# Performance work log

Hardware: AMD Instinct MI355X
Metric: run time of the kernel (lower is better)

The kernel has to match this reference:

```python
import jax, jax.numpy as jnp
import numpy as np

EPS = 1e-08

def _compute_W(V, C, eps=EPS):
    # W = H_k ... H_1, applied sequentially as in the torch loop
    W = jnp.eye(C, dtype=V.dtype)
    def step(W, v):
        v = v / (jnp.linalg.norm(v) + eps)
        # H @ W = W - 2 v (v^T W)
        W = W - 2.0 * jnp.outer(v, v @ W)
        return W, None
    W, _ = jax.lax.scan(step, W, V)
    return W

def setup_inputs() -> dict:
    key = jax.random.key(0)
    k1, k2 = jax.random.split(key)
    x = jax.random.normal(k1, (16, 512, 64, 64), dtype=jnp.float32)
    V = jax.random.normal(k2, (32, 512), dtype=jnp.float32)
    return {"x": x, "V": V}

def reference(x, V):
    B, C, H, Wd = x.shape
    W = _compute_W(V, C)  # [C, C] orthogonal
    # 1x1 conv: out[b,o,h,w] = sum_c W[o,c] * x[b,c,h,w]
    return jnp.einsum('oc,bchw->bohw', W, x)
```

## Files before the change

### kernel.cpp

```cpp
#include <hip/hip_runtime.h>
#include <hip/hip_bf16.h>
#include <stdint.h>
#include <stddef.h>

#define HH_EPS 1e-8f

typedef __attribute__((ext_vector_type(8))) short short8;
typedef __attribute__((ext_vector_type(4))) float f32x4;

#define CDIM 512
#define SDIM 4096
#define BN 128
#define BK 32
#define NSTEP 16

__device__ __forceinline__ size_t wt_idx(int o, int c) {
    return ((((size_t)(c >> 5) * 4 + (o >> 7)) * 8 + ((o >> 4) & 7)) * 64
            + (size_t)((c >> 3) & 3) * 16 + (o & 15)) * 8 + (c & 7);
}

__global__ void compute_w(const float* __restrict__ V,
                          __hip_bfloat16* __restrict__ Wt) {
    const int wave = threadIdx.x >> 6;
    const int lane = threadIdx.x & 63;
    const int jA = (blockIdx.x * 4 + wave) * 2;
    const int jB = jA + 1;
    const int ib = lane * 8;

    float wA[8], wB[8];
    #pragma unroll
    for (int r = 0; r < 8; r++) {
        wA[r] = (ib + r == jA) ? 1.0f : 0.0f;
        wB[r] = (ib + r == jB) ? 1.0f : 0.0f;
    }
    float4 c0 = *(const float4*)(V + ib);
    float4 c1 = *(const float4*)(V + ib + 4);

    for (int k = 0; k < 32; k++) {
        const float v[8] = {c0.x, c0.y, c0.z, c0.w, c1.x, c1.y, c1.z, c1.w};
        if (k < 31) {
            c0 = *(const float4*)(V + (size_t)(k + 1) * 512 + ib);
            c1 = *(const float4*)(V + (size_t)(k + 1) * 512 + ib + 4);
        }
        float dA = 0.0f, dB = 0.0f, ss = 0.0f;
        #pragma unroll
        for (int r = 0; r < 8; r++) {
            dA += v[r] * wA[r];
            dB += v[r] * wB[r];
            ss += v[r] * v[r];
        }
        #pragma unroll
        for (int off = 32; off > 0; off >>= 1) {
            dA += __shfl_xor(dA, off);
            dB += __shfl_xor(dB, off);
            ss += __shfl_xor(ss, off);
        }
        const float t = sqrtf(ss) + HH_EPS;
        const float scale = 2.0f / (t * t);
        const float tA = scale * dA, tB = scale * dB;
        #pragma unroll
        for (int r = 0; r < 8; r++) {
            wA[r] -= tA * v[r];
            wB[r] -= tB * v[r];
        }
    }
    #pragma unroll
    for (int r = 0; r < 8; r++) {
        Wt[wt_idx(ib + r, jA)] = __float2bfloat16(wA[r]);
        Wt[wt_idx(ib + r, jB)] = __float2bfloat16(wB[r]);
    }
}

__device__ __forceinline__ void gld_lds16(const void* g, void* l) {
    __builtin_amdgcn_global_load_lds(
        (const __attribute__((address_space(1))) uint32_t*)g,
        (__attribute__((address_space(3))) uint32_t*)l, 16, 0, 0);
}

template<int N> __device__ __forceinline__ void wait_vm() {
    __builtin_amdgcn_s_waitcnt((N & 15) | ((N >> 4) << 14) | (7 << 4) | (15 << 8));
}

__device__ __forceinline__ void lds_barrier() {
    __builtin_amdgcn_s_waitcnt(0xC07F);
    __builtin_amdgcn_s_barrier();
}

constexpr int vm_pre(int kt) { return (kt + 4 < NSTEP) ? 8 : 0; }

__global__ __launch_bounds__(512, 2) void hh_gemm(
    const float* __restrict__ x,
    const __hip_bfloat16* __restrict__ Wt,
    float* __restrict__ out)
{
    __shared__ __attribute__((aligned(16))) __hip_bfloat16 Albuf[2][CDIM * BK];
    __shared__ __attribute__((aligned(16))) __hip_bfloat16 Bbuf[2][BN * BK];

    const int tid  = threadIdx.x;
    const int wave = tid >> 6, lane = tid & 63;
    const int ow = wave & 3, nh = wave >> 2;
    const int quad = lane >> 4, l16 = lane & 15;

    const int bid = blockIdx.x;
    const int b   = bid >> 5;
    const int nt  = bid & 31;
    const int n0  = nt * BN;

    const float* xb = x + (size_t)b * CDIM * SDIM;
    const int bn = tid & 127;
    const int kq = tid >> 7;
    const float* xp0 = xb + (size_t)(kq * 8) * SDIM + n0 + bn;

    f32x4 acc[4][8];
    #pragma unroll
    for (int mi = 0; mi < 4; mi++)
        #pragma unroll
        for (int oi = 0; oi < 8; oi++) {
            f32x4 z = {0.0f, 0.0f, 0.0f, 0.0f};
            acc[mi][oi] = z;
        }

    float pfB[4][8];

    auto loadA = [&](int kt, int p) {
        const char* gbase = (const char*)Wt
            + ((size_t)(kt * 4 + ow) * 8 + nh * 4) * 1024 + (size_t)lane * 16;
        char* lbase = (char*)&Albuf[p][0] + (size_t)(ow * 8 + nh * 4) * 1024;
        #pragma unroll
        for (int i = 0; i < 4; i++)
            gld_lds16(gbase + (size_t)i * 1024, lbase + (size_t)i * 1024);
    };
    auto loadB = [&](int kt, float* dst) {
        const float* p = xp0 + (size_t)kt * BK * SDIM;
        #pragma unroll
        for (int j = 0; j < 8; j++)
            dst[j] = __builtin_nontemporal_load(p + (size_t)j * SDIM);
    };
    auto writeB = [&](int buf, const float* src) {
        short8 pk;
        #pragma unroll
        for (int j = 0; j < 8; j++) {
            __hip_bfloat16 h = __float2bfloat16(src[j]);
            pk[j] = *(short*)&h;
        }
        *(short8*)(&Bbuf[buf][(size_t)(((bn >> 4) * 4 + kq) * 16 + (bn & 15)) * 8]) = pk;
    };

    loadA(0, 0);
    loadB(0, pfB[0]);
    loadB(1, pfB[1]);
    loadB(2, pfB[2]);
    loadB(3, pfB[3]);
    writeB(0, pfB[0]);
    wait_vm<24>();
    lds_barrier();

#define DO_STEP(KT)                                                            \
    {                                                                          \
        constexpr int p = (KT) & 1;                                            \
        if constexpr ((KT) + 1 < NSTEP) loadA((KT) + 1, p ^ 1);                \
        if constexpr ((KT) + 4 < NSTEP) loadB((KT) + 4, pfB[(KT) % 4]);        \
        short8 afr[4], bfr[8];                                                 \
        _Pragma("unroll")                                                      \
        for (int mi = 0; mi < 4; mi++)                                         \
            afr[mi] = *(const short8*)(&Bbuf[p][(size_t)((nh * 4 + mi) * 64    \
                                                         + lane) * 8]);       \
        _Pragma("unroll")                                                      \
        for (int oi = 0; oi < 8; oi++)                                         \
            bfr[oi] = *(const short8*)(&Albuf[p][(size_t)((ow * 8 + oi) * 64   \
                                                          + lane) * 8]);      \
        _Pragma("unroll")                                                      \
        for (int mi = 0; mi < 4; mi++)                                         \
            _Pragma("unroll")                                                  \
            for (int oi = 0; oi < 8; oi++)                                     \
                acc[mi][oi] = __builtin_amdgcn_mfma_f32_16x16x32_bf16(         \
                    afr[mi], bfr[oi], acc[mi][oi], 0, 0, 0);                   \
        if constexpr ((KT) + 1 < NSTEP) {                                      \
            writeB(p ^ 1, pfB[((KT) + 1) % 4]);                                \
            wait_vm<vm_pre(KT)>();    \
            lds_barrier();                    \
        }                                                                      \
    }

    DO_STEP(0)  DO_STEP(1)  DO_STEP(2)  DO_STEP(3)
    DO_STEP(4)  DO_STEP(5)  DO_STEP(6)  DO_STEP(7)
    DO_STEP(8)  DO_STEP(9)  DO_STEP(10) DO_STEP(11)
    DO_STEP(12) DO_STEP(13) DO_STEP(14) DO_STEP(15)
#undef DO_STEP

    float* ob = out + (size_t)b * CDIM * SDIM + n0 + nh * 64;
    #pragma unroll
    for (int oi = 0; oi < 8; oi++) {
        const int o = ow * 128 + oi * 16 + l16;
        #pragma unroll
        for (int mi = 0; mi < 4; mi++) {
            f32x4* dst = (f32x4*)(ob + (size_t)o * SDIM + mi * 16 + quad * 4);
            __builtin_nontemporal_store(acc[mi][oi], dst);
        }
    }
}

extern "C" void kernel_launch(void* const* d_in, const int* in_sizes, int n_in,
                              void* d_out, int out_size, void* d_ws, size_t ws_size,
                              hipStream_t stream) {
    const float* x = (const float*)d_in[0];
    const float* V = (const float*)d_in[1];
    float* out = (float*)d_out;

    __hip_bfloat16* Wt = (__hip_bfloat16*)d_ws;

    compute_w<<<64, 256, 0, stream>>>(V, Wt);
    hh_gemm<<<512, 512, 0, stream>>>(x, Wt, out);
}
```

Measured before the change: 275.2 us.

## Split GEMM tile into half-output blocks with smaller spatial tile

```diff
diff --git a/kernel.cpp b/kernel.cpp
--- a/kernel.cpp
+++ b/kernel.cpp
@@ -10,12 +10,13 @@
 
 #define CDIM 512
 #define SDIM 4096
-#define BN 128
+#define BM 256
+#define BN 64
 #define BK 32
 #define NSTEP 16
 
 __device__ __forceinline__ size_t wt_idx(int o, int c) {
-    return ((((size_t)(c >> 5) * 4 + (o >> 7)) * 8 + ((o >> 4) & 7)) * 64
+    return (((size_t)(c >> 5) * 32 + (o >> 4)) * 64
             + (size_t)((c >> 3) & 3) * 16 + (o & 15)) * 8 + (c & 7);
 }
 
@@ -86,46 +87,47 @@
     __builtin_amdgcn_s_barrier();
 }
 
-constexpr int vm_pre(int kt) { return (kt + 4 < NSTEP) ? 8 : 0; }
-
-__global__ __launch_bounds__(512, 2) void hh_gemm(
+constexpr int vm_pre(int kt) { return (kt + 3 < NSTEP) ? 8 : 0; }
+
+__global__ __launch_bounds__(256, 3) void hh_gemm(
     const float* __restrict__ x,
     const __hip_bfloat16* __restrict__ Wt,
     float* __restrict__ out)
 {
-    __shared__ __attribute__((aligned(16))) __hip_bfloat16 Albuf[2][CDIM * BK];
+    __shared__ __attribute__((aligned(16))) __hip_bfloat16 Albuf[2][BM * BK];
     __shared__ __attribute__((aligned(16))) __hip_bfloat16 Bbuf[2][BN * BK];
 
     const int tid  = threadIdx.x;
     const int wave = tid >> 6, lane = tid & 63;
-    const int ow = wave & 3, nh = wave >> 2;
+    const int ow = wave;
     const int quad = lane >> 4, l16 = lane & 15;
 
     const int bid = blockIdx.x;
-    const int b   = bid >> 5;
-    const int nt  = bid & 31;
+    const int op  = bid & 1;
+    const int nt  = (bid >> 1) & 63;
+    const int b   = bid >> 7;
     const int n0  = nt * BN;
 
     const float* xb = x + (size_t)b * CDIM * SDIM;
-    const int bn = tid & 127;
-    const int kq = tid >> 7;
+    const int bn = tid & 63;
+    const int kq = wave;
     const float* xp0 = xb + (size_t)(kq * 8) * SDIM + n0 + bn;
 
-    f32x4 acc[4][8];
+    f32x4 acc[4][4];
     #pragma unroll
     for (int mi = 0; mi < 4; mi++)
         #pragma unroll
-        for (int oi = 0; oi < 8; oi++) {
+        for (int oi = 0; oi < 4; oi++) {
             f32x4 z = {0.0f, 0.0f, 0.0f, 0.0f};
             acc[mi][oi] = z;
         }
 
-    float pfB[4][8];
+    float pfB[3][8];
 
     auto loadA = [&](int kt, int p) {
         const char* gbase = (const char*)Wt
-            + ((size_t)(kt * 4 + ow) * 8 + nh * 4) * 1024 + (size_t)lane * 16;
-        char* lbase = (char*)&Albuf[p][0] + (size_t)(ow * 8 + nh * 4) * 1024;
+            + ((size_t)kt * 32 + op * 16 + ow * 4) * 1024 + (size_t)lane * 16;
+        char* lbase = (char*)&Albuf[p][0] + (size_t)(ow * 4) * 1024;
         #pragma unroll
         for (int i = 0; i < 4; i++)
             gld_lds16(gbase + (size_t)i * 1024, lbase + (size_t)i * 1024);
@@ -133,8 +135,7 @@
     auto loadB = [&](int kt, float* dst) {
         const float* p = xp0 + (size_t)kt * BK * SDIM;
         #pragma unroll
-        for (int j = 0; j < 8; j++)
-            dst[j] = __builtin_nontemporal_load(p + (size_t)j * SDIM);
+        for (int j = 0; j < 8; j++) dst[j] = p[(size_t)j * SDIM];
     };
     auto writeB = [&](int buf, const float* src) {
         short8 pk;
@@ -150,35 +151,33 @@
     loadB(0, pfB[0]);
     loadB(1, pfB[1]);
     loadB(2, pfB[2]);
-    loadB(3, pfB[3]);
     writeB(0, pfB[0]);
-    wait_vm<24>();
+    wait_vm<16>();
     lds_barrier();
 
 #define DO_STEP(KT)                                                            \
     {                                                                          \
         constexpr int p = (KT) & 1;                                            \
         if constexpr ((KT) + 1 < NSTEP) loadA((KT) + 1, p ^ 1);                \
-        if constexpr ((KT) + 4 < NSTEP) loadB((KT) + 4, pfB[(KT) % 4]);        \
-        short8 afr[4], bfr[8];                                                 \
+        if constexpr ((KT) + 3 < NSTEP) loadB((KT) + 3, pfB[(KT) % 3]);        \
+        short8 afr[4], bfr[4];                                                 \
         _Pragma("unroll")                                                      \
         for (int mi = 0; mi < 4; mi++)                                         \
-            afr[mi] = *(const short8*)(&Bbuf[p][(size_t)((nh * 4 + mi) * 64    \
-                                                         + lane) * 8]);       \
+            afr[mi] = *(const short8*)(&Bbuf[p][(size_t)(mi * 64 + lane) * 8]);\
         _Pragma("unroll")                                                      \
-        for (int oi = 0; oi < 8; oi++)                                         \
-            bfr[oi] = *(const short8*)(&Albuf[p][(size_t)((ow * 8 + oi) * 64   \
+        for (int oi = 0; oi < 4; oi++)                                         \
+            bfr[oi] = *(const short8*)(&Albuf[p][(size_t)((ow * 4 + oi) * 64   \
                                                           + lane) * 8]);      \
         _Pragma("unroll")                                                      \
         for (int mi = 0; mi < 4; mi++)                                         \
             _Pragma("unroll")                                                  \
-            for (int oi = 0; oi < 8; oi++)                                     \
+            for (int oi = 0; oi < 4; oi++)                                     \
                 acc[mi][oi] = __builtin_amdgcn_mfma_f32_16x16x32_bf16(         \
                     afr[mi], bfr[oi], acc[mi][oi], 0, 0, 0);                   \
         if constexpr ((KT) + 1 < NSTEP) {                                      \
-            writeB(p ^ 1, pfB[((KT) + 1) % 4]);                                \
-            wait_vm<vm_pre(KT)>();    \
-            lds_barrier();                    \
+            writeB(p ^ 1, pfB[((KT) + 1) % 3]);                                \
+            wait_vm<vm_pre(KT)>();  \
+            lds_barrier();                                                     \
         }                                                                      \
     }
 
@@ -188,14 +187,13 @@
     DO_STEP(12) DO_STEP(13) DO_STEP(14) DO_STEP(15)
 #undef DO_STEP
 
-    float* ob = out + (size_t)b * CDIM * SDIM + n0 + nh * 64;
-    #pragma unroll
-    for (int oi = 0; oi < 8; oi++) {
-        const int o = ow * 128 + oi * 16 + l16;
+    float* ob = out + (size_t)b * CDIM * SDIM + n0;
+    #pragma unroll
+    for (int oi = 0; oi < 4; oi++) {
+        const int o = op * 256 + ow * 64 + oi * 16 + l16;
         #pragma unroll
         for (int mi = 0; mi < 4; mi++) {
-            f32x4* dst = (f32x4*)(ob + (size_t)o * SDIM + mi * 16 + quad * 4);
-            __builtin_nontemporal_store(acc[mi][oi], dst);
+            *(f32x4*)(ob + (size_t)o * SDIM + mi * 16 + quad * 4) = acc[mi][oi];
         }
     }
 }
@@ -210,5 +208,5 @@
     __hip_bfloat16* Wt = (__hip_bfloat16*)d_ws;
 
     compute_w<<<64, 256, 0, stream>>>(V, Wt);
-    hh_gemm<<<512, 512, 0, stream>>>(x, Wt, out);
-}
+    hh_gemm<<<2048, 256, 0, stream>>>(x, Wt, out);
+}
```

New measurement: 280.1 us. No clear change (+1.8%).
